# Kernel tuning notes

Hardware: AMD Instinct MI355X
Metric: run time of the kernel (lower is better)

## Reference

```python
import jax, jax.numpy as jnp
import numpy as np

NEG_SLOPE_ATTN = 0.2   # DGL GATConv attention leaky_relu slope
NEG_SLOPE_ACT = 0.01   # nn.LeakyReLU() default activation slope


def _gat_layer(h, src, dst, W, al, ar, b, activate):
    """One DGL-style GATConv. h: [N, F_in]; W: [F_in, H*D]; al/ar: [H, D]; b: [H*D].
    Returns [N, H, D]."""
    N = h.shape[0]
    H, D = al.shape
    feat = (h @ W).reshape(N, H, D)                      # [N, H, D]
    el = jnp.sum(feat * al, axis=-1)                     # [N, H] source term
    er = jnp.sum(feat * ar, axis=-1)                     # [N, H] dest term
    e = jax.nn.leaky_relu(el[src] + er[dst], NEG_SLOPE_ATTN)  # [E, H]
    # segment softmax over destination nodes
    m = jax.ops.segment_max(e, dst, num_segments=N)      # [N, H]
    ex = jnp.exp(e - m[dst])                             # [E, H]
    s = jax.ops.segment_sum(ex, dst, num_segments=N)     # [N, H]
    alpha = ex / s[dst]                                  # [E, H]
    msg = feat[src] * alpha[..., None]                   # [E, H, D]
    out = jax.ops.segment_sum(msg, dst, num_segments=N)  # [N, H, D]
    out = out + b.reshape(H, D)
    if activate:
        out = jax.nn.leaky_relu(out, NEG_SLOPE_ACT)
    return out


def setup_inputs() -> dict:
    key = jax.random.key(0)
    ks = jax.random.split(key, 16)
    N, E, IN = 50000, 800000, 128
    H, D = 2, 128
    HD = H * D
    lin = lambda k, fi, fo: (jax.random.normal(k, (fi, fo), jnp.float32) / np.sqrt(fi).astype(np.float32))
    att = lambda k, h, d: jax.random.normal(k, (h, d), jnp.float32) * 0.1
    return {
        "features": jax.random.normal(ks[0], (N, IN), jnp.float32),
        "src": jax.random.randint(ks[1], (E,), 0, N),
        "dst": jax.random.randint(ks[2], (E,), 0, N),
        "W0": lin(ks[3], IN, HD), "al0": att(ks[4], H, D), "ar0": att(ks[5], H, D), "b0": jnp.zeros((HD,), jnp.float32),
        "W1": lin(ks[6], HD, HD), "al1": att(ks[7], H, D), "ar1": att(ks[8], H, D), "b1": jnp.zeros((HD,), jnp.float32),
        "W2": lin(ks[9], HD, 1), "al2": att(ks[10], 1, 1), "ar2": att(ks[11], 1, 1), "b2": jnp.zeros((1,), jnp.float32),
    }


def reference(features, src, dst, W0, al0, ar0, b0, W1, al1, ar1, b1, W2, al2, ar2, b2):
    N = features.shape[0]
    # hidden GAT layers with head flattening (dropout is identity in eval mode)
    h = _gat_layer(features, src, dst, W0, al0, ar0, b0, True).reshape(N, -1)
    h = _gat_layer(h, src, dst, W1, al1, ar1, b1, True).reshape(N, -1)
    # final single-head, out_feats=1, no activation
    out = _gat_layer(h, src, dst, W2, al2, ar2, b2, False)  # [N, 1, 1]
    return out.squeeze(), h
```

## Files before the change

kernel.cpp:

```cpp
#include <hip/hip_runtime.h>
#include <hip/hip_fp16.h>
#include <math.h>


#define NEG_ATTN 0.2f
#define NEG_ACT  0.01f

typedef short bf16x8 __attribute__((ext_vector_type(8)));
typedef float f32x4  __attribute__((ext_vector_type(4)));


__global__ void count_edges(const int* __restrict__ dst, int* __restrict__ counts, int E) {
    int e = blockIdx.x * blockDim.x + threadIdx.x;
    if (e < E) atomicAdd(&counts[dst[e]], 1);
}

__global__ void scan_offsets(const int* __restrict__ counts, int* __restrict__ offsets, int N) {
    const int PER = 16;
    __shared__ int tmp[1024];
    __shared__ int carry_sh;
    int t = threadIdx.x;
    if (t == 0) { carry_sh = 0; offsets[0] = 0; }
    __syncthreads();
    for (int base = 0; base < N; base += 1024 * PER) {
        int i0 = base + t * PER;
        int loc[PER];
        int sum = 0;
        #pragma unroll
        for (int j = 0; j < PER; ++j) {
            int i = i0 + j;
            int v = (i < N) ? counts[i] : 0;
            sum += v;
            loc[j] = sum;
        }
        tmp[t] = sum;
        __syncthreads();
        for (int off = 1; off < 1024; off <<= 1) {
            int x = (t >= off) ? tmp[t - off] : 0;
            __syncthreads();
            tmp[t] += x;
            __syncthreads();
        }
        int excl = (t == 0) ? 0 : tmp[t - 1];
        int carry = carry_sh;
        #pragma unroll
        for (int j = 0; j < PER; ++j) {
            int i = i0 + j;
            if (i < N) offsets[i + 1] = carry + excl + loc[j];
        }
        __syncthreads();
        if (t == 0) carry_sh = carry + tmp[1023];
        __syncthreads();
    }
}

__global__ void scatter_edges(const int* __restrict__ src, const int* __restrict__ dst,
                              const int* __restrict__ offsets, int* __restrict__ cursor,
                              int* __restrict__ csr_src, int E) {
    int e = blockIdx.x * blockDim.x + threadIdx.x;
    if (e < E) {
        int d = dst[e];
        int pos = offsets[d] + atomicAdd(&cursor[d], 1);
        csr_src[pos] = src[e];
    }
}


__global__ void transpose_w_bf16(const float* __restrict__ W,
                                 unsigned short* __restrict__ Wt_hi,
                                 unsigned short* __restrict__ Wt_lo, int K, int Nw) {
    int idx = blockIdx.x * blockDim.x + threadIdx.x;
    if (idx >= K * Nw) return;
    int k = idx / Nw, n = idx - k * Nw;
    float x = W[idx];
    unsigned bits = __float_as_uint(x);
    unsigned short hh = (unsigned short)(bits >> 16);
    float hf = __uint_as_float(bits & 0xFFFF0000u);
    float lo = x - hf;
    Wt_hi[(size_t)n * K + k] = hh;
    Wt_lo[(size_t)n * K + k] = (unsigned short)(__float_as_uint(lo) >> 16);
}


__global__ __launch_bounds__(256) void gemm_mfma_fused(
    const float* __restrict__ A,
    const unsigned short* __restrict__ Bt_hi, const unsigned short* __restrict__ Bt_lo,
    const float* __restrict__ alf, const float* __restrict__ arf,
    __half* __restrict__ feat16, float* __restrict__ el, float* __restrict__ er,
    int M, int K)
{
    const int BK = 32, LDT = 40;
    __shared__ unsigned short As_hi[64][LDT], As_lo[64][LDT];
    __shared__ unsigned short Bs_hi[64][LDT], Bs_lo[64][LDT];

    int tid = threadIdx.x, wv = tid >> 6, lane = tid & 63;
    int bm = blockIdx.x * 64, bn = blockIdx.y * 64;
    int wr = wv >> 1, wc = wv & 1;

    f32x4 acc[2][2] = {};

    int srow = tid >> 2;
    int skc  = (tid & 3) * 8;

    int arow_g = min(bm + srow, M - 1);
    const float* Arow = A + (size_t)arow_g * K;
    const unsigned short* Bh = Bt_hi + (size_t)(bn + srow) * K;
    const unsigned short* Bl = Bt_lo + (size_t)(bn + srow) * K;

    int frow = lane & 15;
    int fkg  = (lane >> 4) * 8;

    for (int k0 = 0; k0 < K; k0 += BK) {
        float4 v0 = *reinterpret_cast<const float4*>(&Arow[k0 + skc]);
        float4 v1 = *reinterpret_cast<const float4*>(&Arow[k0 + skc + 4]);
        float xs[8] = {v0.x, v0.y, v0.z, v0.w, v1.x, v1.y, v1.z, v1.w};
        unsigned hp[4], lp[4];
        #pragma unroll
        for (int j = 0; j < 4; ++j) {
            unsigned b0 = __float_as_uint(xs[2*j]);
            unsigned b1 = __float_as_uint(xs[2*j+1]);
            float h0 = __uint_as_float(b0 & 0xFFFF0000u);
            float h1 = __uint_as_float(b1 & 0xFFFF0000u);
            unsigned l0 = __float_as_uint(xs[2*j] - h0) >> 16;
            unsigned l1 = __float_as_uint(xs[2*j+1] - h1) >> 16;
            hp[j] = (b0 >> 16) | (b1 & 0xFFFF0000u);
            lp[j] = l0 | (l1 << 16);
        }
        *reinterpret_cast<uint4*>(&As_hi[srow][skc]) = make_uint4(hp[0], hp[1], hp[2], hp[3]);
        *reinterpret_cast<uint4*>(&As_lo[srow][skc]) = make_uint4(lp[0], lp[1], lp[2], lp[3]);
        *reinterpret_cast<uint4*>(&Bs_hi[srow][skc]) =
            *reinterpret_cast<const uint4*>(&Bh[k0 + skc]);
        *reinterpret_cast<uint4*>(&Bs_lo[srow][skc]) =
            *reinterpret_cast<const uint4*>(&Bl[k0 + skc]);

        __syncthreads();

        bf16x8 ah[2], al_[2], bh[2], bl[2];
        #pragma unroll
        for (int i = 0; i < 2; ++i) {
            int r = wr * 32 + i * 16 + frow;
            ah[i]  = *reinterpret_cast<const bf16x8*>(&As_hi[r][fkg]);
            al_[i] = *reinterpret_cast<const bf16x8*>(&As_lo[r][fkg]);
        }
        #pragma unroll
        for (int j = 0; j < 2; ++j) {
            int r = wc * 32 + j * 16 + frow;
            bh[j] = *reinterpret_cast<const bf16x8*>(&Bs_hi[r][fkg]);
            bl[j] = *reinterpret_cast<const bf16x8*>(&Bs_lo[r][fkg]);
        }
        #pragma unroll
        for (int i = 0; i < 2; ++i)
            #pragma unroll
            for (int j = 0; j < 2; ++j) {
                acc[i][j] = __builtin_amdgcn_mfma_f32_16x16x32_bf16(ah[i],  bh[j], acc[i][j], 0, 0, 0);
                acc[i][j] = __builtin_amdgcn_mfma_f32_16x16x32_bf16(ah[i],  bl[j], acc[i][j], 0, 0, 0);
                acc[i][j] = __builtin_amdgcn_mfma_f32_16x16x32_bf16(al_[i], bh[j], acc[i][j], 0, 0, 0);
            }

        __syncthreads();
    }

    int colbase = bn + wc * 32;
    int c0 = colbase + (lane & 15);
    int c1 = c0 + 16;
    float alw0 = alf[c0], alw1 = alf[c1];
    float arw0 = arf[c0], arw1 = arf[c1];
    int hH = colbase >> 7;
    int g4 = (lane >> 4) * 4;
    int sub = lane & 15;

    #pragma unroll
    for (int i = 0; i < 2; ++i) {
        int row0 = bm + wr * 32 + i * 16 + g4;
        #pragma unroll
        for (int r = 0; r < 4; ++r) {
            int row = row0 + r;
            if (row < M) {
                feat16[(size_t)row * 256 + c0] = __float2half(acc[i][0][r]);
                feat16[(size_t)row * 256 + c1] = __float2half(acc[i][1][r]);
            }
        }
        float pel[4], per_[4];
        #pragma unroll
        for (int r = 0; r < 4; ++r) {
            pel[r]  = acc[i][0][r] * alw0 + acc[i][1][r] * alw1;
            per_[r] = acc[i][0][r] * arw0 + acc[i][1][r] * arw1;
        }
        #pragma unroll
        for (int off = 1; off < 16; off <<= 1) {
            #pragma unroll
            for (int r = 0; r < 4; ++r) {
                pel[r]  += __shfl_xor(pel[r], off);
                per_[r] += __shfl_xor(per_[r], off);
            }
        }
        if (sub < 4) {
            int row = row0 + sub;
            float v = (sub == 0) ? pel[0] : (sub == 1) ? pel[1] : (sub == 2) ? pel[2] : pel[3];
            if (row < M) atomicAdd(&el[(size_t)row * 2 + hH], v);
        } else if (sub < 8) {
            int r = sub - 4;
            int row = row0 + r;
            float v = (r == 0) ? per_[0] : (r == 1) ? per_[1] : (r == 2) ? per_[2] : per_[3];
            if (row < M) atomicAdd(&er[(size_t)row * 2 + hH], v);
        }
    }
}


__global__ __launch_bounds__(256) void gat_fused_agg(
    const __half* __restrict__ feat16, const float* __restrict__ el, const float* __restrict__ er,
    const int* __restrict__ offsets, const int* __restrict__ csr_src,
    const float* __restrict__ bias, float* __restrict__ out, int N, int activate,
    const float* __restrict__ W2, float* __restrict__ feat2)
{
    int wv = threadIdx.x >> 6, lane = threadIdx.x & 63;
    int n = blockIdx.x * 4 + wv;
    if (n >= N) return;
    int hsel = lane >> 5;
    int d4 = (lane & 31) * 4 + hsel * 128;
    const char* fbase = (const char*)feat16 + (size_t)d4 * 2;
    int p0 = offsets[n], p1 = offsets[n + 1];

    float2 ern = *reinterpret_cast<const float2*>(er + 2 * (size_t)n);
    const float NEG_INF = -__builtin_inff();
    float m0 = NEG_INF, m1 = NEG_INF, s0 = 0.f, s1 = 0.f;
    float4 acc = make_float4(0.f, 0.f, 0.f, 0.f);

    for (int base = p0; base < p1; base += 32) {
        int cnt = min(32, p1 - base);
        int cl = lane & 31;
        bool active = cl < cnt;
        int src_v = csr_src[base + min(cl, cnt - 1)];
        float ex = NEG_INF, ey = NEG_INF;
        if (active) {
            float2 e2 = *reinterpret_cast<const float2*>(el + 2 * (size_t)src_v);
            ex = e2.x + ern.x; ey = e2.y + ern.y;
            ex = (ex >= 0.f) ? ex : NEG_ATTN * ex;
            ey = (ey >= 0.f) ? ey : NEG_ATTN * ey;
        }
        float mc0 = ex, mc1 = ey;
        #pragma unroll
        for (int off = 16; off; off >>= 1) {
            mc0 = fmaxf(mc0, __shfl_xor(mc0, off));
            mc1 = fmaxf(mc1, __shfl_xor(mc1, off));
        }
        float nm0 = fmaxf(m0, mc0), nm1 = fmaxf(m1, mc1);
        float sc0 = __expf(m0 - nm0), sc1 = __expf(m1 - nm1);
        float wx = active ? __expf(ex - nm0) : 0.f;
        float wy = active ? __expf(ey - nm1) : 0.f;
        float sw0 = wx, sw1 = wy;
        #pragma unroll
        for (int off = 16; off; off >>= 1) {
            sw0 += __shfl_xor(sw0, off);
            sw1 += __shfl_xor(sw1, off);
        }
        s0 = s0 * sc0 + sw0;
        s1 = s1 * sc1 + sw1;
        float scH = hsel ? sc1 : sc0;
        acc.x *= scH; acc.y *= scH; acc.z *= scH; acc.w *= scH;
        m0 = nm0; m1 = nm1;

        int c = 0;
        for (; c + 4 <= cnt; c += 4) {
            int   i0 = __shfl(src_v, c);
            int   i1 = __shfl(src_v, c + 1);
            int   i2 = __shfl(src_v, c + 2);
            int   i3 = __shfl(src_v, c + 3);
            float ax0 = __shfl(wx, c),     ay0 = __shfl(wy, c);
            float ax1 = __shfl(wx, c + 1), ay1 = __shfl(wy, c + 1);
            float ax2 = __shfl(wx, c + 2), ay2 = __shfl(wy, c + 2);
            float ax3 = __shfl(wx, c + 3), ay3 = __shfl(wy, c + 3);
            float a0 = hsel ? ay0 : ax0;
            float a1 = hsel ? ay1 : ax1;
            float a2 = hsel ? ay2 : ax2;
            float a3 = hsel ? ay3 : ax3;
            uint2 r0 = *reinterpret_cast<const uint2*>(fbase + (size_t)i0 * 512);
            uint2 r1 = *reinterpret_cast<const uint2*>(fbase + (size_t)i1 * 512);
            uint2 r2 = *reinterpret_cast<const uint2*>(fbase + (size_t)i2 * 512);
            uint2 r3 = *reinterpret_cast<const uint2*>(fbase + (size_t)i3 * 512);
            {
                float2 fa = __half22float2(*reinterpret_cast<const __half2*>(&r0.x));
                float2 fb = __half22float2(*reinterpret_cast<const __half2*>(&r0.y));
                acc.x = fmaf(a0, fa.x, acc.x); acc.y = fmaf(a0, fa.y, acc.y);
                acc.z = fmaf(a0, fb.x, acc.z); acc.w = fmaf(a0, fb.y, acc.w);
            }
            {
                float2 fa = __half22float2(*reinterpret_cast<const __half2*>(&r1.x));
                float2 fb = __half22float2(*reinterpret_cast<const __half2*>(&r1.y));
                acc.x = fmaf(a1, fa.x, acc.x); acc.y = fmaf(a1, fa.y, acc.y);
                acc.z = fmaf(a1, fb.x, acc.z); acc.w = fmaf(a1, fb.y, acc.w);
            }
            {
                float2 fa = __half22float2(*reinterpret_cast<const __half2*>(&r2.x));
                float2 fb = __half22float2(*reinterpret_cast<const __half2*>(&r2.y));
                acc.x = fmaf(a2, fa.x, acc.x); acc.y = fmaf(a2, fa.y, acc.y);
                acc.z = fmaf(a2, fb.x, acc.z); acc.w = fmaf(a2, fb.y, acc.w);
            }
            {
                float2 fa = __half22float2(*reinterpret_cast<const __half2*>(&r3.x));
                float2 fb = __half22float2(*reinterpret_cast<const __half2*>(&r3.y));
                acc.x = fmaf(a3, fa.x, acc.x); acc.y = fmaf(a3, fa.y, acc.y);
                acc.z = fmaf(a3, fb.x, acc.z); acc.w = fmaf(a3, fb.y, acc.w);
            }
        }
        for (; c < cnt; ++c) {
            int   i0 = __shfl(src_v, c);
            float ax0 = __shfl(wx, c), ay0 = __shfl(wy, c);
            float a0 = hsel ? ay0 : ax0;
            uint2 r0 = *reinterpret_cast<const uint2*>(fbase + (size_t)i0 * 512);
            float2 fa = __half22float2(*reinterpret_cast<const __half2*>(&r0.x));
            float2 fb = __half22float2(*reinterpret_cast<const __half2*>(&r0.y));
            acc.x = fmaf(a0, fa.x, acc.x); acc.y = fmaf(a0, fa.y, acc.y);
            acc.z = fmaf(a0, fb.x, acc.z); acc.w = fmaf(a0, fb.y, acc.w);
        }
    }

    float inv0 = (s0 > 0.f) ? 1.f / s0 : 0.f;
    float inv1 = (s1 > 0.f) ? 1.f / s1 : 0.f;
    float inv = hsel ? inv1 : inv0;
    float4 b4 = *reinterpret_cast<const float4*>(bias + d4);
    acc.x = fmaf(acc.x, inv, b4.x);
    acc.y = fmaf(acc.y, inv, b4.y);
    acc.z = fmaf(acc.z, inv, b4.z);
    acc.w = fmaf(acc.w, inv, b4.w);
    if (activate) {
        acc.x = (acc.x >= 0.f) ? acc.x : NEG_ACT * acc.x;
        acc.y = (acc.y >= 0.f) ? acc.y : NEG_ACT * acc.y;
        acc.z = (acc.z >= 0.f) ? acc.z : NEG_ACT * acc.z;
        acc.w = (acc.w >= 0.f) ? acc.w : NEG_ACT * acc.w;
    }
    *reinterpret_cast<float4*>(out + (size_t)n * 256 + d4) = acc;

    if (W2 != nullptr) {
        float4 w4 = *reinterpret_cast<const float4*>(W2 + d4);
        float d = acc.x * w4.x + acc.y * w4.y + acc.z * w4.z + acc.w * w4.w;
        #pragma unroll
        for (int off = 32; off; off >>= 1) d += __shfl_xor(d, off);
        if (lane == 0) feat2[n] = d;
    }
}


__global__ __launch_bounds__(256) void gat_aggregate2_wave(
    const float* __restrict__ feat2, const float* __restrict__ al2, const float* __restrict__ ar2,
    const float* __restrict__ b2, const int* __restrict__ offsets, const int* __restrict__ csr_src,
    float* __restrict__ out, int N)
{
    int wv = threadIdx.x >> 6, lane = threadIdx.x & 63;
    int n = blockIdx.x * 4 + wv;
    if (n >= N) return;
    float alv = al2[0], arv = ar2[0];
    float ern = feat2[n] * arv;
    int p0 = offsets[n], p1 = offsets[n + 1];
    const float NEG_INF = -__builtin_inff();
    float m = NEG_INF, s = 0.f, acc = 0.f;

    for (int base = p0; base < p1; base += 64) {
        bool active = (base + lane) < p1;
        int sn = active ? csr_src[base + lane] : 0;
        float f = active ? feat2[sn] : 0.f;
        float e = NEG_INF;
        if (active) {
            e = fmaf(f, alv, ern);
            e = (e >= 0.f) ? e : NEG_ATTN * e;
        }
        float mc = e;
        #pragma unroll
        for (int off = 32; off; off >>= 1) mc = fmaxf(mc, __shfl_xor(mc, off));
        float nm = fmaxf(m, mc);
        float sc = __expf(m - nm);
        float w = active ? __expf(e - nm) : 0.f;
        s   = s * sc + w;
        acc = acc * sc + w * f;
        m = nm;
    }
    #pragma unroll
    for (int off = 32; off; off >>= 1) {
        s   += __shfl_xor(s, off);
        acc += __shfl_xor(acc, off);
    }
    if (lane == 0) out[n] = ((s > 0.f) ? acc / s : 0.f) + b2[0];
}


extern "C" void kernel_launch(void* const* d_in, const int* in_sizes, int n_in,
                              void* d_out, int out_size, void* d_ws, size_t ws_size,
                              hipStream_t stream)
{
    const float* features = (const float*)d_in[0];
    const int*   src      = (const int*)d_in[1];
    const int*   dst      = (const int*)d_in[2];
    const float* W0  = (const float*)d_in[3];
    const float* al0 = (const float*)d_in[4];
    const float* ar0 = (const float*)d_in[5];
    const float* b0  = (const float*)d_in[6];
    const float* W1  = (const float*)d_in[7];
    const float* al1 = (const float*)d_in[8];
    const float* ar1 = (const float*)d_in[9];
    const float* b1  = (const float*)d_in[10];
    const float* W2  = (const float*)d_in[11];
    const float* al2 = (const float*)d_in[12];
    const float* ar2 = (const float*)d_in[13];
    const float* b2  = (const float*)d_in[14];

    const int IN = 128, HD = 256;
    const int N = in_sizes[0] / IN;
    const int E = in_sizes[1];

    float* out_final = (float*)d_out;
    float* h2        = (float*)d_out + N;

    char* ws = (char*)d_ws;
    size_t off = 0;
    auto alloc = [&](size_t bytes) { void* p = ws + off; off += (bytes + 255) & ~255ULL; return p; };
    __half* featH  = (__half*)alloc((size_t)N * HD * 2);
    float*  el     = (float*)alloc((size_t)N * 2 * 4);
    float*  er     = (float*)alloc((size_t)N * 2 * 4);
    float*  feat2  = (float*)alloc((size_t)N * 4);
    int*    counts = (int*)alloc((size_t)N * 4);
    int*    cursor = (int*)alloc((size_t)N * 4);
    int*    offs   = (int*)alloc((size_t)(N + 1) * 4);
    int*    csr_src = (int*)alloc((size_t)E * 4);
    unsigned short* Wt0h = (unsigned short*)alloc((size_t)IN * HD * 2);
    unsigned short* Wt0l = (unsigned short*)alloc((size_t)IN * HD * 2);
    unsigned short* Wt1h = (unsigned short*)alloc((size_t)HD * HD * 2);
    unsigned short* Wt1l = (unsigned short*)alloc((size_t)HD * HD * 2);

    hipMemsetAsync(counts, 0, (size_t)N * 4, stream);
    hipMemsetAsync(cursor, 0, (size_t)N * 4, stream);

    transpose_w_bf16<<<(IN * HD + 255) / 256, 256, 0, stream>>>(W0, Wt0h, Wt0l, IN, HD);
    transpose_w_bf16<<<(HD * HD + 255) / 256, 256, 0, stream>>>(W1, Wt1h, Wt1l, HD, HD);

    count_edges<<<(E + 255) / 256, 256, 0, stream>>>(dst, counts, E);
    scan_offsets<<<1, 1024, 0, stream>>>(counts, offs, N);
    scatter_edges<<<(E + 255) / 256, 256, 0, stream>>>(src, dst, offs, cursor, csr_src, E);

    dim3 gemm_grid((N + 63) / 64, HD / 64);

    hipMemsetAsync(el, 0, (size_t)N * 2 * 4, stream);
    hipMemsetAsync(er, 0, (size_t)N * 2 * 4, stream);
    gemm_mfma_fused<<<gemm_grid, 256, 0, stream>>>(features, Wt0h, Wt0l, al0, ar0,
                                                   featH, el, er, N, IN);
    gat_fused_agg<<<(N + 3) / 4, 256, 0, stream>>>(featH, el, er, offs, csr_src, b0,
                                                   h2, N, 1, nullptr, nullptr);

    hipMemsetAsync(el, 0, (size_t)N * 2 * 4, stream);
    hipMemsetAsync(er, 0, (size_t)N * 2 * 4, stream);
    gemm_mfma_fused<<<gemm_grid, 256, 0, stream>>>(h2, Wt1h, Wt1l, al1, ar1,
                                                   featH, el, er, N, HD);
    gat_fused_agg<<<(N + 3) / 4, 256, 0, stream>>>(featH, el, er, offs, csr_src, b1,
                                                   h2, N, 1, W2, feat2);

    gat_aggregate2_wave<<<(N + 3) / 4, 256, 0, stream>>>(feat2, al2, ar2, b2, offs,
                                                         csr_src, out_final, N);
}
```

Baseline: 473.4 us.

## Pre-split GEMM inputs to bf16 hi/lo, widen K tile, parallelize offset scan

Replaces the single-block serial prefix scan with a three-phase multi-block scan. The GEMM no longer loads fp32 A and splits it into bf16 hi/lo per tile. A separate pass splits the input features, and the first aggregation kernel writes layer-1 outputs already split. The GEMM K tile grows from 32 to 64 to halve synchronisations. This adds an extra features pass and extra hi/lo global writes in exchange for cheaper GEMM inner loops and a parallel scan.

Measured after the change: 434.7 us. 8.2% less time.

```diff
diff --git a/kernel.cpp b/kernel.cpp
--- a/kernel.cpp
+++ b/kernel.cpp
@@ -8,6 +8,14 @@
 
 typedef short bf16x8 __attribute__((ext_vector_type(8)));
 typedef float f32x4  __attribute__((ext_vector_type(4)));
+typedef unsigned short ushort_t;
+
+__device__ inline void bf16split(float x, unsigned short& h, unsigned short& l) {
+    unsigned b = __float_as_uint(x);
+    h = (unsigned short)(b >> 16);
+    float hf = __uint_as_float(b & 0xFFFF0000u);
+    l = (unsigned short)(__float_as_uint(x - hf) >> 16);
+}
 
 
 __global__ void count_edges(const int* __restrict__ dst, int* __restrict__ counts, int E) {
@@ -15,43 +23,54 @@
     if (e < E) atomicAdd(&counts[dst[e]], 1);
 }
 
-__global__ void scan_offsets(const int* __restrict__ counts, int* __restrict__ offsets, int N) {
-    const int PER = 16;
-    __shared__ int tmp[1024];
-    __shared__ int carry_sh;
+__global__ __launch_bounds__(256) void scan_phase1(
+    const int* __restrict__ in, int* __restrict__ out1 ,
+    int* __restrict__ bsum, int n)
+{
+    __shared__ int wsum[4];
+    int i = blockIdx.x * 256 + threadIdx.x;
+    int lane = threadIdx.x & 63, wv = threadIdx.x >> 6;
+    int v = (i < n) ? in[i] : 0;
+    int x = v;
+    #pragma unroll
+    for (int off = 1; off < 64; off <<= 1) {
+        int y = __shfl_up(x, off);
+        if (lane >= off) x += y;
+    }
+    if (lane == 63) wsum[wv] = x;
+    __syncthreads();
+    int add = 0;
+    for (int w = 0; w < wv; ++w) add += wsum[w];
+    x += add;
+    if (i < n) out1[i] = x;
+    if (threadIdx.x == 255) bsum[blockIdx.x] = x;
+}
+
+__global__ __launch_bounds__(256) void scan_phase2(int* __restrict__ bsum, int nb) {
+    __shared__ int wsum[4];
     int t = threadIdx.x;
-    if (t == 0) { carry_sh = 0; offsets[0] = 0; }
+    int lane = t & 63, wv = t >> 6;
+    int x = (t < nb) ? bsum[t] : 0;
+    #pragma unroll
+    for (int off = 1; off < 64; off <<= 1) {
+        int y = __shfl_up(x, off);
+        if (lane >= off) x += y;
+    }
+    if (lane == 63) wsum[wv] = x;
     __syncthreads();
-    for (int base = 0; base < N; base += 1024 * PER) {
-        int i0 = base + t * PER;
-        int loc[PER];
-        int sum = 0;
-        #pragma unroll
-        for (int j = 0; j < PER; ++j) {
-            int i = i0 + j;
-            int v = (i < N) ? counts[i] : 0;
-            sum += v;
-            loc[j] = sum;
-        }
-        tmp[t] = sum;
-        __syncthreads();
-        for (int off = 1; off < 1024; off <<= 1) {
-            int x = (t >= off) ? tmp[t - off] : 0;
-            __syncthreads();
-            tmp[t] += x;
-            __syncthreads();
-        }
-        int excl = (t == 0) ? 0 : tmp[t - 1];
-        int carry = carry_sh;
-        #pragma unroll
-        for (int j = 0; j < PER; ++j) {
-            int i = i0 + j;
-            if (i < N) offsets[i + 1] = carry + excl + loc[j];
-        }
-        __syncthreads();
-        if (t == 0) carry_sh = carry + tmp[1023];
-        __syncthreads();
-    }
+    int add = 0;
+    for (int w = 0; w < wv; ++w) add += wsum[w];
+    x += add;
+    if (t < nb) bsum[t] = x;
+}
+
+__global__ __launch_bounds__(256) void scan_phase3(
+    int* __restrict__ out1, const int* __restrict__ bsum, int n)
+{
+    int i = blockIdx.x * 256 + threadIdx.x;
+    int add = (blockIdx.x > 0) ? bsum[blockIdx.x - 1] : 0;
+    if (i < n) out1[i] += add;
+    if (i == 0) out1[-1] = 0;
 }
 
 __global__ void scatter_edges(const int* __restrict__ src, const int* __restrict__ dst,
@@ -67,31 +86,43 @@
 
 
 __global__ void transpose_w_bf16(const float* __restrict__ W,
-                                 unsigned short* __restrict__ Wt_hi,
-                                 unsigned short* __restrict__ Wt_lo, int K, int Nw) {
+                                 ushort_t* __restrict__ Wt_hi,
+                                 ushort_t* __restrict__ Wt_lo, int K, int Nw) {
     int idx = blockIdx.x * blockDim.x + threadIdx.x;
     if (idx >= K * Nw) return;
     int k = idx / Nw, n = idx - k * Nw;
-    float x = W[idx];
-    unsigned bits = __float_as_uint(x);
-    unsigned short hh = (unsigned short)(bits >> 16);
-    float hf = __uint_as_float(bits & 0xFFFF0000u);
-    float lo = x - hf;
-    Wt_hi[(size_t)n * K + k] = hh;
-    Wt_lo[(size_t)n * K + k] = (unsigned short)(__float_as_uint(lo) >> 16);
-}
-
-
-__global__ __launch_bounds__(256) void gemm_mfma_fused(
-    const float* __restrict__ A,
-    const unsigned short* __restrict__ Bt_hi, const unsigned short* __restrict__ Bt_lo,
+    unsigned short h, l;
+    bf16split(W[idx], h, l);
+    Wt_hi[(size_t)n * K + k] = h;
+    Wt_lo[(size_t)n * K + k] = l;
+}
+
+
+__global__ void split_f32(const float* __restrict__ x,
+                          ushort_t* __restrict__ hi, ushort_t* __restrict__ lo, int n4) {
+    int i = blockIdx.x * blockDim.x + threadIdx.x;
+    if (i >= n4) return;
+    float4 v = reinterpret_cast<const float4*>(x)[i];
+    ushort4 h, l;
+    bf16split(v.x, h.x, l.x);
+    bf16split(v.y, h.y, l.y);
+    bf16split(v.z, h.z, l.z);
+    bf16split(v.w, h.w, l.w);
+    reinterpret_cast<ushort4*>(hi)[i] = h;
+    reinterpret_cast<ushort4*>(lo)[i] = l;
+}
+
+
+__global__ __launch_bounds__(256) void gemm_bf16split(
+    const ushort_t* __restrict__ Ah, const ushort_t* __restrict__ Al,
+    const ushort_t* __restrict__ Bh, const ushort_t* __restrict__ Bl,
     const float* __restrict__ alf, const float* __restrict__ arf,
     __half* __restrict__ feat16, float* __restrict__ el, float* __restrict__ er,
     int M, int K)
 {
-    const int BK = 32, LDT = 40;
-    __shared__ unsigned short As_hi[64][LDT], As_lo[64][LDT];
-    __shared__ unsigned short Bs_hi[64][LDT], Bs_lo[64][LDT];
+    const int LDT = 72;
+    __shared__ ushort_t As_hi[64][LDT], As_lo[64][LDT];
+    __shared__ ushort_t Bs_hi[64][LDT], Bs_lo[64][LDT];
 
     int tid = threadIdx.x, wv = tid >> 6, lane = tid & 63;
     int bm = blockIdx.x * 64, bn = blockIdx.y * 64;
@@ -100,63 +131,54 @@
     f32x4 acc[2][2] = {};
 
     int srow = tid >> 2;
-    int skc  = (tid & 3) * 8;
-
-    int arow_g = min(bm + srow, M - 1);
-    const float* Arow = A + (size_t)arow_g * K;
-    const unsigned short* Bh = Bt_hi + (size_t)(bn + srow) * K;
-    const unsigned short* Bl = Bt_lo + (size_t)(bn + srow) * K;
+    int sc0  = (tid & 3) * 16;
+
+    size_t abase = (size_t)min(bm + srow, M - 1) * K;
+    size_t bbase = (size_t)(bn + srow) * K;
 
     int frow = lane & 15;
     int fkg  = (lane >> 4) * 8;
 
-    for (int k0 = 0; k0 < K; k0 += BK) {
-        float4 v0 = *reinterpret_cast<const float4*>(&Arow[k0 + skc]);
-        float4 v1 = *reinterpret_cast<const float4*>(&Arow[k0 + skc + 4]);
-        float xs[8] = {v0.x, v0.y, v0.z, v0.w, v1.x, v1.y, v1.z, v1.w};
-        unsigned hp[4], lp[4];
-        #pragma unroll
-        for (int j = 0; j < 4; ++j) {
-            unsigned b0 = __float_as_uint(xs[2*j]);
-            unsigned b1 = __float_as_uint(xs[2*j+1]);
-            float h0 = __uint_as_float(b0 & 0xFFFF0000u);
-            float h1 = __uint_as_float(b1 & 0xFFFF0000u);
-            unsigned l0 = __float_as_uint(xs[2*j] - h0) >> 16;
-            unsigned l1 = __float_as_uint(xs[2*j+1] - h1) >> 16;
-            hp[j] = (b0 >> 16) | (b1 & 0xFFFF0000u);
-            lp[j] = l0 | (l1 << 16);
-        }
-        *reinterpret_cast<uint4*>(&As_hi[srow][skc]) = make_uint4(hp[0], hp[1], hp[2], hp[3]);
-        *reinterpret_cast<uint4*>(&As_lo[srow][skc]) = make_uint4(lp[0], lp[1], lp[2], lp[3]);
-        *reinterpret_cast<uint4*>(&Bs_hi[srow][skc]) =
-            *reinterpret_cast<const uint4*>(&Bh[k0 + skc]);
-        *reinterpret_cast<uint4*>(&Bs_lo[srow][skc]) =
-            *reinterpret_cast<const uint4*>(&Bl[k0 + skc]);
-
+    for (int k0 = 0; k0 < K; k0 += 64) {
+        #pragma unroll
+        for (int j = 0; j < 2; ++j) {
+            int c = sc0 + j * 8;
+            *reinterpret_cast<uint4*>(&As_hi[srow][c]) =
+                *reinterpret_cast<const uint4*>(&Ah[abase + k0 + c]);
+            *reinterpret_cast<uint4*>(&As_lo[srow][c]) =
+                *reinterpret_cast<const uint4*>(&Al[abase + k0 + c]);
+            *reinterpret_cast<uint4*>(&Bs_hi[srow][c]) =
+                *reinterpret_cast<const uint4*>(&Bh[bbase + k0 + c]);
+            *reinterpret_cast<uint4*>(&Bs_lo[srow][c]) =
+                *reinterpret_cast<const uint4*>(&Bl[bbase + k0 + c]);
+        }
         __syncthreads();
 
-        bf16x8 ah[2], al_[2], bh[2], bl[2];
-        #pragma unroll
-        for (int i = 0; i < 2; ++i) {
-            int r = wr * 32 + i * 16 + frow;
-            ah[i]  = *reinterpret_cast<const bf16x8*>(&As_hi[r][fkg]);
-            al_[i] = *reinterpret_cast<const bf16x8*>(&As_lo[r][fkg]);
-        }
-        #pragma unroll
-        for (int j = 0; j < 2; ++j) {
-            int r = wc * 32 + j * 16 + frow;
-            bh[j] = *reinterpret_cast<const bf16x8*>(&Bs_hi[r][fkg]);
-            bl[j] = *reinterpret_cast<const bf16x8*>(&Bs_lo[r][fkg]);
-        }
-        #pragma unroll
-        for (int i = 0; i < 2; ++i)
+        #pragma unroll
+        for (int ks = 0; ks < 2; ++ks) {
+            int kb = ks * 32 + fkg;
+            bf16x8 ah[2], al_[2], bh[2], bl[2];
+            #pragma unroll
+            for (int i = 0; i < 2; ++i) {
+                int r = wr * 32 + i * 16 + frow;
+                ah[i]  = *reinterpret_cast<const bf16x8*>(&As_hi[r][kb]);
+                al_[i] = *reinterpret_cast<const bf16x8*>(&As_lo[r][kb]);
+            }
             #pragma unroll
             for (int j = 0; j < 2; ++j) {
-                acc[i][j] = __builtin_amdgcn_mfma_f32_16x16x32_bf16(ah[i],  bh[j], acc[i][j], 0, 0, 0);
-                acc[i][j] = __builtin_amdgcn_mfma_f32_16x16x32_bf16(ah[i],  bl[j], acc[i][j], 0, 0, 0);
-                acc[i][j] = __builtin_amdgcn_mfma_f32_16x16x32_bf16(al_[i], bh[j], acc[i][j], 0, 0, 0);
-            }
-
+                int r = wc * 32 + j * 16 + frow;
+                bh[j] = *reinterpret_cast<const bf16x8*>(&Bs_hi[r][kb]);
+                bl[j] = *reinterpret_cast<const bf16x8*>(&Bs_lo[r][kb]);
+            }
+            #pragma unroll
+            for (int i = 0; i < 2; ++i)
+                #pragma unroll
+                for (int j = 0; j < 2; ++j) {
+                    acc[i][j] = __builtin_amdgcn_mfma_f32_16x16x32_bf16(ah[i],  bh[j], acc[i][j], 0, 0, 0);
+                    acc[i][j] = __builtin_amdgcn_mfma_f32_16x16x32_bf16(ah[i],  bl[j], acc[i][j], 0, 0, 0);
+                    acc[i][j] = __builtin_amdgcn_mfma_f32_16x16x32_bf16(al_[i], bh[j], acc[i][j], 0, 0, 0);
+                }
+        }
         __syncthreads();
     }
 
@@ -212,7 +234,8 @@
     const __half* __restrict__ feat16, const float* __restrict__ el, const float* __restrict__ er,
     const int* __restrict__ offsets, const int* __restrict__ csr_src,
     const float* __restrict__ bias, float* __restrict__ out, int N, int activate,
-    const float* __restrict__ W2, float* __restrict__ feat2)
+    const float* __restrict__ W2, float* __restrict__ feat2,
+    ushort_t* __restrict__ outHi, ushort_t* __restrict__ outLo)
 {
     int wv = threadIdx.x >> 6, lane = threadIdx.x & 63;
     int n = blockIdx.x * 4 + wv;
@@ -332,6 +355,16 @@
     }
     *reinterpret_cast<float4*>(out + (size_t)n * 256 + d4) = acc;
 
+    if (outHi != nullptr) {
+        ushort4 h, l;
+        bf16split(acc.x, h.x, l.x);
+        bf16split(acc.y, h.y, l.y);
+        bf16split(acc.z, h.z, l.z);
+        bf16split(acc.w, h.w, l.w);
+        *reinterpret_cast<ushort4*>(outHi + (size_t)n * 256 + d4) = h;
+        *reinterpret_cast<ushort4*>(outLo + (size_t)n * 256 + d4) = l;
+    }
+
     if (W2 != nullptr) {
         float4 w4 = *reinterpret_cast<const float4*>(W2 + d4);
         float d = acc.x * w4.x + acc.y * w4.y + acc.z * w4.z + acc.w * w4.w;
@@ -407,6 +440,7 @@
     const int IN = 128, HD = 256;
     const int N = in_sizes[0] / IN;
     const int E = in_sizes[1];
+    const int NB = (N + 255) / 256;
 
     float* out_final = (float*)d_out;
     float* h2        = (float*)d_out + N;
@@ -414,44 +448,52 @@
     char* ws = (char*)d_ws;
     size_t off = 0;
     auto alloc = [&](size_t bytes) { void* p = ws + off; off += (bytes + 255) & ~255ULL; return p; };
-    __half* featH  = (__half*)alloc((size_t)N * HD * 2);
-    float*  el     = (float*)alloc((size_t)N * 2 * 4);
-    float*  er     = (float*)alloc((size_t)N * 2 * 4);
-    float*  feat2  = (float*)alloc((size_t)N * 4);
-    int*    counts = (int*)alloc((size_t)N * 4);
-    int*    cursor = (int*)alloc((size_t)N * 4);
-    int*    offs   = (int*)alloc((size_t)(N + 1) * 4);
-    int*    csr_src = (int*)alloc((size_t)E * 4);
-    unsigned short* Wt0h = (unsigned short*)alloc((size_t)IN * HD * 2);
-    unsigned short* Wt0l = (unsigned short*)alloc((size_t)IN * HD * 2);
-    unsigned short* Wt1h = (unsigned short*)alloc((size_t)HD * HD * 2);
-    unsigned short* Wt1l = (unsigned short*)alloc((size_t)HD * HD * 2);
+    __half*   featH  = (__half*)alloc((size_t)N * HD * 2);
+    ushort_t* Fh     = (ushort_t*)alloc((size_t)N * IN * 2);
+    ushort_t* Fl     = (ushort_t*)alloc((size_t)N * IN * 2);
+    ushort_t* H1h    = (ushort_t*)alloc((size_t)N * HD * 2);
+    ushort_t* H1l    = (ushort_t*)alloc((size_t)N * HD * 2);
+    float*    el     = (float*)alloc((size_t)N * 2 * 4);
+    float*    er     = (float*)alloc((size_t)N * 2 * 4);
+    float*    feat2  = (float*)alloc((size_t)N * 4);
+    int*      counts = (int*)alloc((size_t)N * 4);
+    int*      cursor = (int*)alloc((size_t)N * 4);
+    int*      offs   = (int*)alloc((size_t)(N + 1) * 4);
+    int*      bsum   = (int*)alloc((size_t)NB * 4);
+    int*      csr_src = (int*)alloc((size_t)E * 4);
+    ushort_t* Wt0h = (ushort_t*)alloc((size_t)IN * HD * 2);
+    ushort_t* Wt0l = (ushort_t*)alloc((size_t)IN * HD * 2);
+    ushort_t* Wt1h = (ushort_t*)alloc((size_t)HD * HD * 2);
+    ushort_t* Wt1l = (ushort_t*)alloc((size_t)HD * HD * 2);
 
     hipMemsetAsync(counts, 0, (size_t)N * 4, stream);
     hipMemsetAsync(cursor, 0, (size_t)N * 4, stream);
 
     transpose_w_bf16<<<(IN * HD + 255) / 256, 256, 0, stream>>>(W0, Wt0h, Wt0l, IN, HD);
     transpose_w_bf16<<<(HD * HD + 255) / 256, 256, 0, stream>>>(W1, Wt1h, Wt1l, HD, HD);
+    split_f32<<<((N * IN / 4) + 255) / 256, 256, 0, stream>>>(features, Fh, Fl, N * IN / 4);
 
     count_edges<<<(E + 255) / 256, 256, 0, stream>>>(dst, counts, E);
-    scan_offsets<<<1, 1024, 0, stream>>>(counts, offs, N);
+    scan_phase1<<<NB, 256, 0, stream>>>(counts, offs + 1, bsum, N);
+    scan_phase2<<<1, 256, 0, stream>>>(bsum, NB);
+    scan_phase3<<<NB, 256, 0, stream>>>(offs + 1, bsum, N);
     scatter_edges<<<(E + 255) / 256, 256, 0, stream>>>(src, dst, offs, cursor, csr_src, E);
 
     dim3 gemm_grid((N + 63) / 64, HD / 64);
 
     hipMemsetAsync(el, 0, (size_t)N * 2 * 4, stream);
     hipMemsetAsync(er, 0, (size_t)N * 2 * 4, stream);
-    gemm_mfma_fused<<<gemm_grid, 256, 0, stream>>>(features, Wt0h, Wt0l, al0, ar0,
-                                                   featH, el, er, N, IN);
+    gemm_bf16split<<<gemm_grid, 256, 0, stream>>>(Fh, Fl, Wt0h, Wt0l, al0, ar0,
+                                                  featH, el, er, N, IN);
     gat_fused_agg<<<(N + 3) / 4, 256, 0, stream>>>(featH, el, er, offs, csr_src, b0,
-                                                   h2, N, 1, nullptr, nullptr);
+                                                   h2, N, 1, nullptr, nullptr, H1h, H1l);
 
     hipMemsetAsync(el, 0, (size_t)N * 2 * 4, stream);
     hipMemsetAsync(er, 0, (size_t)N * 2 * 4, stream);
-    gemm_mfma_fused<<<gemm_grid, 256, 0, stream>>>(h2, Wt1h, Wt1l, al1, ar1,
-                                                   featH, el, er, N, HD);
+    gemm_bf16split<<<gemm_grid, 256, 0, stream>>>(H1h, H1l, Wt1h, Wt1l, al1, ar1,
+                                                  featH, el, er, N, HD);
     gat_fused_agg<<<(N + 3) / 4, 256, 0, stream>>>(featH, el, er, offs, csr_src, b1,
-                                                   h2, N, 1, W2, feat2);
+                                                   h2, N, 1, W2, feat2, nullptr, nullptr);
 
     gat_aggregate2_wave<<<(N + 3) / 4, 256, 0, stream>>>(feat2, al2, ar2, b2, offs,
                                                          csr_src, out_final, N);
```
